# Optimization experiments

Measured on AMD Instinct MI355X. Metric: run time of the kernel, lower is better.

The kernel has to match this reference:

```python
import jax, jax.numpy as jnp
import numpy as np

D_MODEL = 1024

def setup_inputs() -> dict:
    key = jax.random.key(0)
    ks = jax.random.split(key, 8)
    B, S, D = 8, 2048, D_MODEL
    scale = 1.0 / np.sqrt(D)
    return {
        "x1": jax.random.normal(ks[0], (B, S, D), dtype=jnp.float32),
        "x2": jax.random.normal(ks[1], (B, S, D), dtype=jnp.float32),
        "Wq": jax.random.normal(ks[2], (D, D), dtype=jnp.float32) * scale,
        "bq": jnp.zeros((D,), dtype=jnp.float32),
        "Wk": jax.random.normal(ks[3], (D, D), dtype=jnp.float32) * scale,
        "bk": jnp.zeros((D,), dtype=jnp.float32),
        "Wv": jax.random.normal(ks[4], (D, D), dtype=jnp.float32) * scale,
        "bv": jnp.zeros((D,), dtype=jnp.float32),
    }

def reference(x1, x2, Wq, bq, Wk, bk, Wv, bv):
    # q1: [B, Sq, D]; k2, v2: [B, Sk, D]
    q1 = jnp.einsum('bsd,de->bse', x1, Wq) + bq
    k2 = jnp.einsum('bsd,de->bse', x2, Wk) + bk
    v2 = jnp.einsum('bsd,de->bse', x2, Wv) + bv
    scale = 1.0 / np.sqrt(q1.shape[-1]).astype(np.float32)
    scores = jnp.einsum('bqd,bkd->bqk', q1, k2) * scale  # [B, Sq, Sk]
    probs = jax.nn.softmax(scores, axis=-1)
    return jnp.einsum('bqk,bkd->bqd', probs, v2)
```

## Files before the change

kernel.cpp:

```cpp
#include <hip/hip_runtime.h>
#include <hip/hip_bf16.h>
#include <hip/hip_fp16.h>

typedef __attribute__((ext_vector_type(8))) short short8;
typedef __attribute__((ext_vector_type(4))) float f32x4;

#define DEVI __device__ __forceinline__

DEVI unsigned short f2bf(float f){
  __hip_bfloat16 h = __float2bfloat16(f);
  unsigned short u; __builtin_memcpy(&u, &h, 2); return u;
}

__global__ void cast_f32_bf16(const float* __restrict__ in, unsigned short* __restrict__ out, int n4){
  int stride = gridDim.x * blockDim.x;
  for (int i = blockIdx.x*blockDim.x + threadIdx.x; i < n4; i += stride){
    float4 f = reinterpret_cast<const float4*>(in)[i];
    ushort4 o;
    o.x = f2bf(f.x); o.y = f2bf(f.y); o.z = f2bf(f.z); o.w = f2bf(f.w);
    reinterpret_cast<ushort4*>(out)[i] = o;
  }
}

__global__ void transpose_cast_w(const float* __restrict__ W, unsigned short* __restrict__ WT, int K, int N){
  __shared__ float tile[32][33];
  int bn = blockIdx.x*32, bk = blockIdx.y*32;
  int tx = threadIdx.x & 31, ty = threadIdx.x >> 5;
  for (int r=0;r<32;r+=8)
    tile[ty+r][tx] = W[(long)(bk+ty+r)*N + bn+tx];
  __syncthreads();
  for (int r=0;r<32;r+=8)
    WT[(long)(bn+ty+r)*K + bk+tx] = (short)f2bf(tile[tx][ty+r]);
}

DEVI void stage16(const short* gsrc, short* lbase){
  __builtin_amdgcn_global_load_lds(
      (const __attribute__((address_space(1))) unsigned int*)gsrc,
      (__attribute__((address_space(3))) unsigned int*)lbase, 16, 0, 0);
}

template<int OT, int BIAS>
DEVI void gemm_db_body(const short* __restrict__ A, const short* __restrict__ Bt,
                       const float* __restrict__ bias, void* __restrict__ Cv,
                       int N, int K, long sA, long sB, long sC, float scale, int nx, int ny)
{
  extern __shared__ short lds[];
  const int nwg = gridDim.x;
  const int cpx = nwg >> 3;
  const int wg  = (blockIdx.x & 7)*cpx + (blockIdx.x >> 3);
  const int bx  = wg % nx;
  const int tmp = wg / nx;
  const int by  = tmp % ny;
  const long bz = tmp / ny;
  const int m0 = bx * 128, n0 = by * 128;
  const short* Ab = A  + bz*sA + (long)m0 * K;
  const short* Bb = Bt + bz*sB + (long)n0 * K;

  const int t = threadIdx.x, lane = t & 63, w = t >> 6;
  const int wr = w >> 1, wc = w & 1;

  const int rr = lane >> 2;
  const int kk = ((lane & 3) * 8) ^ ((lane & 32) ? 16 : 0);
  const long off0 = (long)(( w     )*16 + rr) * K + kk;
  const long off1 = (long)(( 4 + w )*16 + rr) * K + kk;

  const int la = lane & 15;
  const int lsw = (la*64 + ((lane>>4)<<4)) ^ ((la>=8)?32:0);
  const short* AP = lds + (lsw>>1) + wr*2048;
  const short* BP = lds + (lsw>>1) + 8192 + wc*2048;

  f32x4 acc[4][4] = {};
  const int NT = K >> 6;

#define STAGEH(BASE, BLK) do {                         \
    stage16((BASE) + off0, (BLK) + w*512);             \
    stage16((BASE) + off1, (BLK) + (4+w)*512);         \
  } while(0)
#define STAGE(BUF, KB) do {                            \
    STAGEH(Ab + (KB),      lds + (BUF)*16384 + 0);     \
    STAGEH(Ab + (KB) + 32, lds + (BUF)*16384 + 4096);  \
    STAGEH(Bb + (KB),      lds + (BUF)*16384 + 8192);  \
    STAGEH(Bb + (KB) + 32, lds + (BUF)*16384 + 12288); \
  } while(0)

  STAGE(0, 0);
  STAGE(1, 64);
  asm volatile("s_waitcnt vmcnt(8)" ::: "memory");
  asm volatile("s_barrier" ::: "memory");

  int cur = 0;
  for (int u = 0; u < NT; ++u){
    const short* ap = AP + cur*16384;
    const short* bp = BP + cur*16384;
    #pragma unroll
    for (int kh = 0; kh < 2; ++kh){
      short8 b0 = *reinterpret_cast<const short8*>(bp + kh*4096 + 0*512);
      short8 b1 = *reinterpret_cast<const short8*>(bp + kh*4096 + 1*512);
      short8 b2 = *reinterpret_cast<const short8*>(bp + kh*4096 + 2*512);
      short8 b3 = *reinterpret_cast<const short8*>(bp + kh*4096 + 3*512);
      short8 a0 = *reinterpret_cast<const short8*>(ap + kh*4096 + 0*512);
      short8 a1 = *reinterpret_cast<const short8*>(ap + kh*4096 + 1*512);
      short8 a2 = *reinterpret_cast<const short8*>(ap + kh*4096 + 2*512);
      short8 a3 = *reinterpret_cast<const short8*>(ap + kh*4096 + 3*512);
      acc[0][0] = __builtin_amdgcn_mfma_f32_16x16x32_bf16(a0, b0, acc[0][0],0,0,0);
      acc[0][1] = __builtin_amdgcn_mfma_f32_16x16x32_bf16(a0, b1, acc[0][1],0,0,0);
      acc[0][2] = __builtin_amdgcn_mfma_f32_16x16x32_bf16(a0, b2, acc[0][2],0,0,0);
      acc[0][3] = __builtin_amdgcn_mfma_f32_16x16x32_bf16(a0, b3, acc[0][3],0,0,0);
      acc[1][0] = __builtin_amdgcn_mfma_f32_16x16x32_bf16(a1, b0, acc[1][0],0,0,0);
      acc[1][1] = __builtin_amdgcn_mfma_f32_16x16x32_bf16(a1, b1, acc[1][1],0,0,0);
      acc[1][2] = __builtin_amdgcn_mfma_f32_16x16x32_bf16(a1, b2, acc[1][2],0,0,0);
      acc[1][3] = __builtin_amdgcn_mfma_f32_16x16x32_bf16(a1, b3, acc[1][3],0,0,0);
      acc[2][0] = __builtin_amdgcn_mfma_f32_16x16x32_bf16(a2, b0, acc[2][0],0,0,0);
      acc[2][1] = __builtin_amdgcn_mfma_f32_16x16x32_bf16(a2, b1, acc[2][1],0,0,0);
      acc[2][2] = __builtin_amdgcn_mfma_f32_16x16x32_bf16(a2, b2, acc[2][2],0,0,0);
      acc[2][3] = __builtin_amdgcn_mfma_f32_16x16x32_bf16(a2, b3, acc[2][3],0,0,0);
      acc[3][0] = __builtin_amdgcn_mfma_f32_16x16x32_bf16(a3, b0, acc[3][0],0,0,0);
      acc[3][1] = __builtin_amdgcn_mfma_f32_16x16x32_bf16(a3, b1, acc[3][1],0,0,0);
      acc[3][2] = __builtin_amdgcn_mfma_f32_16x16x32_bf16(a3, b2, acc[3][2],0,0,0);
      acc[3][3] = __builtin_amdgcn_mfma_f32_16x16x32_bf16(a3, b3, acc[3][3],0,0,0);
    }
    asm volatile("s_waitcnt lgkmcnt(0)" ::: "memory");
    asm volatile("s_barrier" ::: "memory");
    int u2 = u + 2; if (u2 >= NT) u2 -= NT;
    STAGE(cur, u2*64);
    asm volatile("s_waitcnt vmcnt(8)" ::: "memory");
    asm volatile("s_barrier" ::: "memory");
    cur ^= 1;
  }
#undef STAGE
#undef STAGEH

  asm volatile("s_waitcnt vmcnt(0)" ::: "memory");

  const int rowb = m0 + wr*64 + ((lane>>4)<<2);
  const int colb = n0 + wc*64 + la;
  #pragma unroll
  for (int m=0;m<4;m++){
    #pragma unroll
    for (int n=0;n<4;n++){
      const int col = colb + n*16;
      float badd = (BIAS==1) ? bias[col] : 0.0f;
      #pragma unroll
      for (int j=0;j<4;j++){
        const int row = rowb + m*16 + j;
        float v = acc[m][n][j] * scale + badd;
        if (BIAS==2) v += bias[row];
        const long idx = bz*sC + (long)row*N + col;
        if constexpr (OT==0) ((float*)Cv)[idx] = v;
        else if constexpr (OT==1) ((__half*)Cv)[idx] = __float2half(v);
        else ((unsigned short*)Cv)[idx] = f2bf(v);
      }
    }
  }
}

#define GATTR __global__ __launch_bounds__(256, 2)
GATTR void g_proj_k(const short* A, const short* Bt, const float* bias, void* Cv,
                    int N, int K, long sA, long sB, long sC, float scale, int nx, int ny)
{ gemm_db_body<2,1>(A,Bt,bias,Cv,N,K,sA,sB,sC,scale,nx,ny); }
GATTR void g_proj_v(const short* A, const short* Bt, const float* bias, void* Cv,
                    int N, int K, long sA, long sB, long sC, float scale, int nx, int ny)
{ gemm_db_body<2,2>(A,Bt,bias,Cv,N,K,sA,sB,sC,scale,nx,ny); }
GATTR void g_proj_q(const short* A, const short* Bt, const float* bias, void* Cv,
                    int N, int K, long sA, long sB, long sC, float scale, int nx, int ny)
{ gemm_db_body<2,1>(A,Bt,bias,Cv,N,K,sA,sB,sC,scale,nx,ny); }
GATTR void g_score(const short* A, const short* Bt, const float* bias, void* Cv,
                   int N, int K, long sA, long sB, long sC, float scale, int nx, int ny)
{ gemm_db_body<1,0>(A,Bt,bias,Cv,N,K,sA,sB,sC,scale,nx,ny); }
GATTR void g_pv(const short* A, const short* Bt, const float* bias, void* Cv,
                int N, int K, long sA, long sB, long sC, float scale, int nx, int ny)
{ gemm_db_body<0,0>(A,Bt,bias,Cv,N,K,sA,sB,sC,scale,nx,ny); }

__global__ void softmax_rows(unsigned short* __restrict__ SP, int cols){
  const long row = blockIdx.x;
  unsigned short* rp = SP + row * cols;
  const int t = threadIdx.x, lane = t & 63, w = t >> 6;
  short8 raw = *reinterpret_cast<const short8*>(rp + t*8);
  float v[8];
  #pragma unroll
  for (int i=0;i<8;i++){
    unsigned short us = (unsigned short)raw[i];
    __half h; __builtin_memcpy(&h, &us, 2);
    v[i] = __half2float(h);
  }
  float m = v[0];
  #pragma unroll
  for (int i=1;i<8;i++) m = fmaxf(m, v[i]);
  #pragma unroll
  for (int o=32;o;o>>=1) m = fmaxf(m, __shfl_down(m, o));
  __shared__ float red[8];
  if (lane==0) red[w] = m;
  __syncthreads();
  if (t==0) red[4] = fmaxf(fmaxf(red[0],red[1]), fmaxf(red[2],red[3]));
  __syncthreads();
  const float rowmax = red[4];
  float s = 0.f;
  #pragma unroll
  for (int i=0;i<8;i++){ v[i] = __expf(v[i]-rowmax); s += v[i]; }
  #pragma unroll
  for (int o=32;o;o>>=1) s += __shfl_down(s, o);
  if (lane==0) red[w] = s;
  __syncthreads();
  if (t==0) red[5] = red[0]+red[1]+red[2]+red[3];
  __syncthreads();
  const float inv = 1.0f / red[5];
  short8 outp;
  #pragma unroll
  for (int i=0;i<8;i++) outp[i] = (short)f2bf(v[i]*inv);
  *reinterpret_cast<short8*>(rp + t*8) = outp;
}

extern "C" void kernel_launch(void* const* d_in, const int* in_sizes, int n_in,
                              void* d_out, int out_size, void* d_ws, size_t ws_size,
                              hipStream_t stream)
{
  const int B = 8, S = 2048, D = 1024;
  const int BS = B * S;
  const float* x1 = (const float*)d_in[0];
  const float* x2 = (const float*)d_in[1];
  const float* Wq = (const float*)d_in[2];
  const float* bq = (const float*)d_in[3];
  const float* Wk = (const float*)d_in[4];
  const float* bk = (const float*)d_in[5];
  const float* Wv = (const float*)d_in[6];
  const float* bv = (const float*)d_in[7];

  char* ws = (char*)d_ws;
  const size_t MB = 1024*1024;
  short*          x1b = (short*)(ws);
  short*          x2b = (short*)(ws + 32*MB);
  unsigned short* Sc  = (unsigned short*)ws;
  short*          q   = (short*)(ws + 64*MB);
  short*          k   = (short*)(ws + 96*MB);
  short*          vT  = (short*)(ws + 128*MB);
  short*          WqT = (short*)(ws + 160*MB);
  short*          WkT = (short*)(ws + 162*MB);
  short*          WvT = (short*)(ws + 164*MB);

  const size_t SH = 65536;

  cast_f32_bf16<<<4096,256,0,stream>>>(x2, (unsigned short*)x2b, BS*D/4);
  transpose_cast_w<<<dim3(32,32),256,0,stream>>>(Wk, (unsigned short*)WkT, D, D);
  transpose_cast_w<<<dim3(32,32),256,0,stream>>>(Wv, (unsigned short*)WvT, D, D);
  g_proj_k<<<1024, 256, SH, stream>>>(x2b, WkT, bk, k, D, D, 0,0,0, 1.0f, 128, 8);
  g_proj_v<<<1024, 256, SH, stream>>>(WvT, x2b, bv, vT, S, D, 0, (long)S*D, (long)D*S, 1.0f, 8, 16);
  cast_f32_bf16<<<4096,256,0,stream>>>(x1, (unsigned short*)x1b, BS*D/4);
  transpose_cast_w<<<dim3(32,32),256,0,stream>>>(Wq, (unsigned short*)WqT, D, D);
  g_proj_q<<<1024, 256, SH, stream>>>(x1b, WqT, bq, q, D, D, 0,0,0, 1.0f, 128, 8);
  g_score<<<2048, 256, SH, stream>>>(q, k, nullptr, Sc, S, D,
                                     (long)S*D, (long)S*D, (long)S*S, 0.03125f, 16, 16);
  softmax_rows<<<BS,256,0,stream>>>(Sc, S);
  g_pv<<<1024, 256, SH, stream>>>((short*)Sc, vT, nullptr, d_out, D, S,
                                  (long)S*S, (long)D*S, (long)S*D, 1.0f, 16, 8);
}
```

Measured before the change: 370.5 us.

## Enlarge GEMM tiles to 256x256 per workgroup with 128x128 per wave

Doubles the block tile of all GEMMs from 128x128 to 256x256, giving each wave an 8x8 grid of MFMA accumulators and doubling LDS staging to 128KB. Grids and launch bounds are adjusted so one workgroup occupies each CU. The aim is higher arithmetic intensity and less global/L2 traffic per FLOP. In exchange it raises register pressure sharply (possible spills) and cuts occupancy, reducing latency hiding.

```diff
diff --git a/kernel.cpp b/kernel.cpp
--- a/kernel.cpp
+++ b/kernel.cpp
@@ -40,7 +40,7 @@
 }
 
 template<int OT, int BIAS>
-DEVI void gemm_db_body(const short* __restrict__ A, const short* __restrict__ Bt,
+DEVI void gemm_ww_body(const short* __restrict__ A, const short* __restrict__ Bt,
                        const float* __restrict__ bias, void* __restrict__ Cv,
                        int N, int K, long sA, long sB, long sC, float scale, int nx, int ny)
 {
@@ -52,7 +52,7 @@
   const int tmp = wg / nx;
   const int by  = tmp % ny;
   const long bz = tmp / ny;
-  const int m0 = bx * 128, n0 = by * 128;
+  const int m0 = bx * 256, n0 = by * 256;
   const short* Ab = A  + bz*sA + (long)m0 * K;
   const short* Bb = Bt + bz*sB + (long)n0 * K;
 
@@ -61,69 +61,59 @@
 
   const int rr = lane >> 2;
   const int kk = ((lane & 3) * 8) ^ ((lane & 32) ? 16 : 0);
-  const long off0 = (long)(( w     )*16 + rr) * K + kk;
-  const long off1 = (long)(( 4 + w )*16 + rr) * K + kk;
+  long off[4];
+  #pragma unroll
+  for (int i=0;i<4;i++) off[i] = (long)((i*4 + w)*16 + rr) * K + kk;
 
   const int la = lane & 15;
   const int lsw = (la*64 + ((lane>>4)<<4)) ^ ((la>=8)?32:0);
-  const short* AP = lds + (lsw>>1) + wr*2048;
-  const short* BP = lds + (lsw>>1) + 8192 + wc*2048;
-
-  f32x4 acc[4][4] = {};
+  const short* APb = lds + (lsw>>1) + wr*4096;
+  const short* BPb = lds + (lsw>>1) + 16384 + wc*4096;
+
+  f32x4 acc[8][8] = {};
   const int NT = K >> 6;
 
-#define STAGEH(BASE, BLK) do {                         \
-    stage16((BASE) + off0, (BLK) + w*512);             \
-    stage16((BASE) + off1, (BLK) + (4+w)*512);         \
+#define STAGEH(BASE, BLK) do {                        \
+    stage16((BASE)+off[0], (BLK)+ w      *512);       \
+    stage16((BASE)+off[1], (BLK)+( 4+w)*512);         \
+    stage16((BASE)+off[2], (BLK)+( 8+w)*512);         \
+    stage16((BASE)+off[3], (BLK)+(12+w)*512);         \
   } while(0)
-#define STAGE(BUF, KB) do {                            \
-    STAGEH(Ab + (KB),      lds + (BUF)*16384 + 0);     \
-    STAGEH(Ab + (KB) + 32, lds + (BUF)*16384 + 4096);  \
-    STAGEH(Bb + (KB),      lds + (BUF)*16384 + 8192);  \
-    STAGEH(Bb + (KB) + 32, lds + (BUF)*16384 + 12288); \
+#define STAGE(BUF, KB) do {                           \
+    STAGEH(Ab+(KB),    lds+(BUF)*32768);              \
+    STAGEH(Ab+(KB)+32, lds+(BUF)*32768+8192);         \
+    STAGEH(Bb+(KB),    lds+(BUF)*32768+16384);        \
+    STAGEH(Bb+(KB)+32, lds+(BUF)*32768+24576);        \
   } while(0)
 
   STAGE(0, 0);
   STAGE(1, 64);
-  asm volatile("s_waitcnt vmcnt(8)" ::: "memory");
+  asm volatile("s_waitcnt vmcnt(16)" ::: "memory");
   asm volatile("s_barrier" ::: "memory");
 
   int cur = 0;
   for (int u = 0; u < NT; ++u){
-    const short* ap = AP + cur*16384;
-    const short* bp = BP + cur*16384;
+    const short* ap = APb + cur*32768;
+    const short* bp = BPb + cur*32768;
     #pragma unroll
     for (int kh = 0; kh < 2; ++kh){
-      short8 b0 = *reinterpret_cast<const short8*>(bp + kh*4096 + 0*512);
-      short8 b1 = *reinterpret_cast<const short8*>(bp + kh*4096 + 1*512);
-      short8 b2 = *reinterpret_cast<const short8*>(bp + kh*4096 + 2*512);
-      short8 b3 = *reinterpret_cast<const short8*>(bp + kh*4096 + 3*512);
-      short8 a0 = *reinterpret_cast<const short8*>(ap + kh*4096 + 0*512);
-      short8 a1 = *reinterpret_cast<const short8*>(ap + kh*4096 + 1*512);
-      short8 a2 = *reinterpret_cast<const short8*>(ap + kh*4096 + 2*512);
-      short8 a3 = *reinterpret_cast<const short8*>(ap + kh*4096 + 3*512);
-      acc[0][0] = __builtin_amdgcn_mfma_f32_16x16x32_bf16(a0, b0, acc[0][0],0,0,0);
-      acc[0][1] = __builtin_amdgcn_mfma_f32_16x16x32_bf16(a0, b1, acc[0][1],0,0,0);
-      acc[0][2] = __builtin_amdgcn_mfma_f32_16x16x32_bf16(a0, b2, acc[0][2],0,0,0);
-      acc[0][3] = __builtin_amdgcn_mfma_f32_16x16x32_bf16(a0, b3, acc[0][3],0,0,0);
-      acc[1][0] = __builtin_amdgcn_mfma_f32_16x16x32_bf16(a1, b0, acc[1][0],0,0,0);
-      acc[1][1] = __builtin_amdgcn_mfma_f32_16x16x32_bf16(a1, b1, acc[1][1],0,0,0);
-      acc[1][2] = __builtin_amdgcn_mfma_f32_16x16x32_bf16(a1, b2, acc[1][2],0,0,0);
-      acc[1][3] = __builtin_amdgcn_mfma_f32_16x16x32_bf16(a1, b3, acc[1][3],0,0,0);
-      acc[2][0] = __builtin_amdgcn_mfma_f32_16x16x32_bf16(a2, b0, acc[2][0],0,0,0);
-      acc[2][1] = __builtin_amdgcn_mfma_f32_16x16x32_bf16(a2, b1, acc[2][1],0,0,0);
-      acc[2][2] = __builtin_amdgcn_mfma_f32_16x16x32_bf16(a2, b2, acc[2][2],0,0,0);
-      acc[2][3] = __builtin_amdgcn_mfma_f32_16x16x32_bf16(a2, b3, acc[2][3],0,0,0);
-      acc[3][0] = __builtin_amdgcn_mfma_f32_16x16x32_bf16(a3, b0, acc[3][0],0,0,0);
-      acc[3][1] = __builtin_amdgcn_mfma_f32_16x16x32_bf16(a3, b1, acc[3][1],0,0,0);
-      acc[3][2] = __builtin_amdgcn_mfma_f32_16x16x32_bf16(a3, b2, acc[3][2],0,0,0);
-      acc[3][3] = __builtin_amdgcn_mfma_f32_16x16x32_bf16(a3, b3, acc[3][3],0,0,0);
+      short8 Af[8], Bf[8];
+      #pragma unroll
+      for (int i=0;i<8;i++) Af[i] = *reinterpret_cast<const short8*>(ap + kh*8192 + i*512);
+      #pragma unroll
+      for (int j=0;j<8;j++) Bf[j] = *reinterpret_cast<const short8*>(bp + kh*8192 + j*512);
+      #pragma unroll
+      for (int i=0;i<8;i++){
+        #pragma unroll
+        for (int j=0;j<8;j++)
+          acc[i][j] = __builtin_amdgcn_mfma_f32_16x16x32_bf16(Af[i], Bf[j], acc[i][j],0,0,0);
+      }
     }
     asm volatile("s_waitcnt lgkmcnt(0)" ::: "memory");
     asm volatile("s_barrier" ::: "memory");
     int u2 = u + 2; if (u2 >= NT) u2 -= NT;
     STAGE(cur, u2*64);
-    asm volatile("s_waitcnt vmcnt(8)" ::: "memory");
+    asm volatile("s_waitcnt vmcnt(16)" ::: "memory");
     asm volatile("s_barrier" ::: "memory");
     cur ^= 1;
   }
@@ -132,18 +122,18 @@
 
   asm volatile("s_waitcnt vmcnt(0)" ::: "memory");
 
-  const int rowb = m0 + wr*64 + ((lane>>4)<<2);
-  const int colb = n0 + wc*64 + la;
-  #pragma unroll
-  for (int m=0;m<4;m++){
+  const int rowb = m0 + wr*128 + ((lane>>4)<<2);
+  const int colb = n0 + wc*128 + la;
+  #pragma unroll
+  for (int mi=0;mi<8;mi++){
     #pragma unroll
-    for (int n=0;n<4;n++){
-      const int col = colb + n*16;
+    for (int nj=0;nj<8;nj++){
+      const int col = colb + nj*16;
       float badd = (BIAS==1) ? bias[col] : 0.0f;
       #pragma unroll
       for (int j=0;j<4;j++){
-        const int row = rowb + m*16 + j;
-        float v = acc[m][n][j] * scale + badd;
+        const int row = rowb + mi*16 + j;
+        float v = acc[mi][nj][j] * scale + badd;
         if (BIAS==2) v += bias[row];
         const long idx = bz*sC + (long)row*N + col;
         if constexpr (OT==0) ((float*)Cv)[idx] = v;
@@ -154,22 +144,22 @@
   }
 }
 
-#define GATTR __global__ __launch_bounds__(256, 2)
+#define GATTR __global__ __launch_bounds__(256, 1)
 GATTR void g_proj_k(const short* A, const short* Bt, const float* bias, void* Cv,
                     int N, int K, long sA, long sB, long sC, float scale, int nx, int ny)
-{ gemm_db_body<2,1>(A,Bt,bias,Cv,N,K,sA,sB,sC,scale,nx,ny); }
+{ gemm_ww_body<2,1>(A,Bt,bias,Cv,N,K,sA,sB,sC,scale,nx,ny); }
 GATTR void g_proj_v(const short* A, const short* Bt, const float* bias, void* Cv,
                     int N, int K, long sA, long sB, long sC, float scale, int nx, int ny)
-{ gemm_db_body<2,2>(A,Bt,bias,Cv,N,K,sA,sB,sC,scale,nx,ny); }
+{ gemm_ww_body<2,2>(A,Bt,bias,Cv,N,K,sA,sB,sC,scale,nx,ny); }
 GATTR void g_proj_q(const short* A, const short* Bt, const float* bias, void* Cv,
                     int N, int K, long sA, long sB, long sC, float scale, int nx, int ny)
-{ gemm_db_body<2,1>(A,Bt,bias,Cv,N,K,sA,sB,sC,scale,nx,ny); }
+{ gemm_ww_body<2,1>(A,Bt,bias,Cv,N,K,sA,sB,sC,scale,nx,ny); }
 GATTR void g_score(const short* A, const short* Bt, const float* bias, void* Cv,
                    int N, int K, long sA, long sB, long sC, float scale, int nx, int ny)
-{ gemm_db_body<1,0>(A,Bt,bias,Cv,N,K,sA,sB,sC,scale,nx,ny); }
+{ gemm_ww_body<1,0>(A,Bt,bias,Cv,N,K,sA,sB,sC,scale,nx,ny); }
 GATTR void g_pv(const short* A, const short* Bt, const float* bias, void* Cv,
                 int N, int K, long sA, long sB, long sC, float scale, int nx, int ny)
-{ gemm_db_body<0,0>(A,Bt,bias,Cv,N,K,sA,sB,sC,scale,nx,ny); }
+{ gemm_ww_body<0,0>(A,Bt,bias,Cv,N,K,sA,sB,sC,scale,nx,ny); }
 
 __global__ void softmax_rows(unsigned short* __restrict__ SP, int cols){
   const long row = blockIdx.x;
@@ -237,19 +227,19 @@
   short*          WkT = (short*)(ws + 162*MB);
   short*          WvT = (short*)(ws + 164*MB);
 
-  const size_t SH = 65536;
+  const size_t SH = 131072;
 
   cast_f32_bf16<<<4096,256,0,stream>>>(x2, (unsigned short*)x2b, BS*D/4);
   transpose_cast_w<<<dim3(32,32),256,0,stream>>>(Wk, (unsigned short*)WkT, D, D);
   transpose_cast_w<<<dim3(32,32),256,0,stream>>>(Wv, (unsigned short*)WvT, D, D);
-  g_proj_k<<<1024, 256, SH, stream>>>(x2b, WkT, bk, k, D, D, 0,0,0, 1.0f, 128, 8);
-  g_proj_v<<<1024, 256, SH, stream>>>(WvT, x2b, bv, vT, S, D, 0, (long)S*D, (long)D*S, 1.0f, 8, 16);
+  g_proj_k<<<256, 256, SH, stream>>>(x2b, WkT, bk, k, D, D, 0,0,0, 1.0f, 64, 4);
+  g_proj_v<<<256, 256, SH, stream>>>(WvT, x2b, bv, vT, S, D, 0, (long)S*D, (long)D*S, 1.0f, 4, 8);
   cast_f32_bf16<<<4096,256,0,stream>>>(x1, (unsigned short*)x1b, BS*D/4);
   transpose_cast_w<<<dim3(32,32),256,0,stream>>>(Wq, (unsigned short*)WqT, D, D);
-  g_proj_q<<<1024, 256, SH, stream>>>(x1b, WqT, bq, q, D, D, 0,0,0, 1.0f, 128, 8);
-  g_score<<<2048, 256, SH, stream>>>(q, k, nullptr, Sc, S, D,
-                                     (long)S*D, (long)S*D, (long)S*S, 0.03125f, 16, 16);
+  g_proj_q<<<256, 256, SH, stream>>>(x1b, WqT, bq, q, D, D, 0,0,0, 1.0f, 64, 4);
+  g_score<<<512, 256, SH, stream>>>(q, k, nullptr, Sc, S, D,
+                                    (long)S*D, (long)S*D, (long)S*S, 0.03125f, 8, 8);
   softmax_rows<<<BS,256,0,stream>>>(Sc, S);
-  g_pv<<<1024, 256, SH, stream>>>((short*)Sc, vT, nullptr, d_out, D, S,
-                                  (long)S*S, (long)D*S, (long)S*D, 1.0f, 16, 8);
-}
+  g_pv<<<256, 256, SH, stream>>>((short*)Sc, vT, nullptr, d_out, D, S,
+                                 (long)S*S, (long)D*S, (long)S*D, 1.0f, 8, 4);
+}
```

Result: slower. 570.7 us (+54.0%).
